# Performance work log

Hardware: AMD Instinct MI355X
Metric: run time of the kernel (lower is better)

## Reference

```python
import jax, jax.numpy as jnp
import numpy as np

D_MODEL = 1024
N_HEADS = 16
HEAD_DIM = D_MODEL // N_HEADS
N_MEM = 16
EPS = 1e-5
ROPE_THETA = 10000.0


def layernorm(x, g, b):
    mu = jnp.mean(x, axis=-1, keepdims=True)
    var = jnp.mean(jnp.square(x - mu), axis=-1, keepdims=True)
    return (x - mu) * jax.lax.rsqrt(var + EPS) * g + b


def rope_cos_sin(seq_len, head_dim, dtype):
    inv_freq = 1.0 / (ROPE_THETA ** (jnp.arange(0, head_dim, 2, dtype=jnp.float32) / head_dim))
    pos = jnp.arange(seq_len, dtype=jnp.float32)
    freqs = pos[:, None] * inv_freq[None, :]            # [S, hd/2]
    emb = jnp.concatenate([freqs, freqs], axis=-1)       # [S, hd]
    return jnp.cos(emb).astype(dtype), jnp.sin(emb).astype(dtype)


def rotate_half(x):
    x1, x2 = jnp.split(x, 2, axis=-1)
    return jnp.concatenate([-x2, x1], axis=-1)


def setup_inputs() -> dict:
    key = jax.random.key(0)
    ks = jax.random.split(key, 8)
    B, T, D = 2, 2048, D_MODEL
    x = jax.random.normal(ks[0], (B, T, D), dtype=jnp.float32)
    memory_tokens = jax.random.normal(ks[1], (1, N_MEM, D), dtype=jnp.float32) * 0.02
    s = 1.0 / np.sqrt(D)
    qkv_w = jax.random.uniform(ks[2], (3 * D, D), minval=-s, maxval=s, dtype=jnp.float32)
    qkv_b = jax.random.uniform(ks[3], (3 * D,), minval=-s, maxval=s, dtype=jnp.float32)
    out_w = jax.random.uniform(ks[4], (D, D), minval=-s, maxval=s, dtype=jnp.float32)
    out_b = jax.random.uniform(ks[5], (D,), minval=-s, maxval=s, dtype=jnp.float32)
    norm_g = jnp.ones((D,), jnp.float32)
    norm_b = jnp.zeros((D,), jnp.float32)
    normm_g = jnp.ones((D,), jnp.float32)
    normm_b = jnp.zeros((D,), jnp.float32)
    return {"x": x, "memory_tokens": memory_tokens, "qkv_w": qkv_w, "qkv_b": qkv_b,
            "out_w": out_w, "out_b": out_b, "norm_g": norm_g, "norm_b": norm_b,
            "normm_g": normm_g, "normm_b": normm_b}


def reference(x, memory_tokens, qkv_w, qkv_b, out_w, out_b, norm_g, norm_b, normm_g, normm_b):
    B, T, D = x.shape
    S = N_MEM + T
    residual = x
    x_norm = layernorm(x, norm_g, norm_b)
    mem = layernorm(jnp.broadcast_to(memory_tokens, (B, N_MEM, D)), normm_g, normm_b)
    xm = jnp.concatenate([mem, x_norm], axis=1)                # [B, S, D]
    qkv = xm @ qkv_w.T + qkv_b                                 # [B, S, 3D]
    qkv = qkv.reshape(B, S, 3, N_HEADS, HEAD_DIM)
    q = jnp.transpose(qkv[:, :, 0], (0, 2, 1, 3))              # [B, H, S, hd]
    k = jnp.transpose(qkv[:, :, 1], (0, 2, 1, 3))
    v = jnp.transpose(qkv[:, :, 2], (0, 2, 1, 3))
    cos, sin = rope_cos_sin(S, HEAD_DIM, x.dtype)              # [S, hd]
    q = q * cos + rotate_half(q) * sin
    k = k * cos + rotate_half(k) * sin
    scale = 1.0 / np.sqrt(HEAD_DIM)
    scores = jnp.einsum("bhqd,bhkd->bhqk", q, k) * scale       # [B, H, S, S]
    causal = jnp.tril(jnp.ones((S, S), dtype=bool))
    scores = jnp.where(causal, scores, jnp.finfo(scores.dtype).min)
    attn = jax.nn.softmax(scores, axis=-1)
    out = jnp.einsum("bhqk,bhkd->bhqd", attn, v)               # [B, H, S, hd]
    out = jnp.transpose(out, (0, 2, 1, 3)).reshape(B, S, D)
    out = out @ out_w.T + out_b
    out = out[:, N_MEM:, :]
    return residual + out
```

## Files before the change

kernel.cpp:

```cpp
#include <hip/hip_runtime.h>
#include <cstdint>


using bf16 = __bf16;
typedef __attribute__((ext_vector_type(8))) __bf16 bf16x8;
typedef __attribute__((ext_vector_type(4))) __bf16 bf16x4;
typedef __attribute__((ext_vector_type(4))) float floatx4;

#define MFMA16(a, b, c) __builtin_amdgcn_mfma_f32_16x16x32_bf16(a, b, c, 0, 0, 0)

constexpr int SV = 2064;
constexpr int SP = 2112;
constexpr float LOG2_THETA = 13.287712379549449f;

__device__ __forceinline__ bool dt_is_bf16(const void* p) {
  return *(const uint32_t*)p == 0x3F803F80u;
}

struct f8 { float v[8]; };

__device__ __forceinline__ f8 load8(const void* p, size_t idx, bool bf) {
  f8 r;
  if (bf) {
    bf16x8 t = *(const bf16x8*)((const bf16*)p + idx);
#pragma unroll
    for (int j = 0; j < 8; ++j) r.v[j] = (float)t[j];
  } else {
    float4 a = *(const float4*)((const float*)p + idx);
    float4 b = *(const float4*)((const float*)p + idx + 4);
    r.v[0] = a.x; r.v[1] = a.y; r.v[2] = a.z; r.v[3] = a.w;
    r.v[4] = b.x; r.v[5] = b.y; r.v[6] = b.z; r.v[7] = b.w;
  }
  return r;
}

__device__ __forceinline__ float ld1(const void* p, size_t idx, bool bf) {
  return bf ? (float)((const bf16*)p)[idx] : ((const float*)p)[idx];
}

__device__ __forceinline__ void load16_to_lds(const bf16* gptr, bf16* lptr) {
  auto* g = reinterpret_cast<const __attribute__((address_space(1))) uint32_t*>(
      reinterpret_cast<uintptr_t>(gptr));
  auto* l = reinterpret_cast<__attribute__((address_space(3))) uint32_t*>(
      reinterpret_cast<uintptr_t>(lptr));
  __builtin_amdgcn_global_load_lds(g, l, 16, 0, 0);
}

__global__ __launch_bounds__(256) void conv_w(
    const void* __restrict__ Wq, const void* __restrict__ Wo,
    const void* __restrict__ flagp, bf16* __restrict__ Wqb,
    bf16* __restrict__ Wob) {
  const bool bf = dt_is_bf16(flagp);
  const size_t i = ((size_t)blockIdx.x * 256 + threadIdx.x) * 8;
  const void* src;
  bf16* dst;
  size_t off;
  if (i < 3145728) { src = Wq; dst = Wqb; off = i; }
  else { src = Wo; dst = Wob; off = i - 3145728; }
  const f8 v = load8(src, off, bf);
  bf16x8 o;
#pragma unroll
  for (int j = 0; j < 8; ++j) o[j] = (bf16)v.v[j];
  *(bf16x8*)&dst[off] = o;
}

__global__ __launch_bounds__(256) void ln_all(
    const void* __restrict__ x, const void* __restrict__ mem,
    const void* __restrict__ ng, const void* __restrict__ nb,
    const void* __restrict__ mg, const void* __restrict__ mb,
    bf16* __restrict__ mem16, bf16* __restrict__ xln) {
  const bool bf = dt_is_bf16(ng);
  const int t = threadIdx.x, wid = t >> 6, lane = t & 63;
  const int row = blockIdx.x * 4 + wid;
  const void *src, *g, *bb;
  size_t soff;
  bf16* out;
  if (row < 16) {
    src = mem; soff = (size_t)row * 1024; g = mg; bb = mb;
    out = mem16 + (size_t)row * 1024;
  } else {
    src = x; soff = (size_t)(row - 16) * 1024; g = ng; bb = nb;
    out = xln + (size_t)(row - 16) * 1024;
  }
  const f8 v0 = load8(src, soff + lane * 8, bf);
  const f8 v1 = load8(src, soff + 512 + lane * 8, bf);
  float sum = 0.f, sq = 0.f;
#pragma unroll
  for (int j = 0; j < 8; ++j) { sum += v0.v[j]; sq += v0.v[j] * v0.v[j]; }
#pragma unroll
  for (int j = 0; j < 8; ++j) { sum += v1.v[j]; sq += v1.v[j] * v1.v[j]; }
#pragma unroll
  for (int off = 1; off < 64; off <<= 1) {
    sum += __shfl_xor(sum, off);
    sq += __shfl_xor(sq, off);
  }
  const float mu = sum * (1.0f / 1024.0f);
  const float var = sq * (1.0f / 1024.0f) - mu * mu;
  const float rstd = rsqrtf(var + 1e-5f);
  const f8 g0 = load8(g, lane * 8, bf), g1 = load8(g, 512 + lane * 8, bf);
  const f8 b0 = load8(bb, lane * 8, bf), b1 = load8(bb, 512 + lane * 8, bf);
  bf16x8 o0, o1;
#pragma unroll
  for (int j = 0; j < 8; ++j) {
    o0[j] = (bf16)((v0.v[j] - mu) * rstd * g0.v[j] + b0.v[j]);
    o1[j] = (bf16)((v1.v[j] - mu) * rstd * g1.v[j] + b1.v[j]);
  }
  *(bf16x8*)&out[lane * 8] = o0;
  *(bf16x8*)&out[512 + lane * 8] = o1;
}

__global__ __launch_bounds__(256) void gemm0_rope(
    const bf16* __restrict__ mem16, const bf16* __restrict__ xln,
    const bf16* __restrict__ Wqb, const void* __restrict__ bias,
    const void* __restrict__ flagp, bf16* __restrict__ Qg,
    bf16* __restrict__ Kg, bf16* __restrict__ Vg) {
  const bool bf = dt_is_bf16(flagp);
  __shared__ bf16 As[128 * 32];
  __shared__ bf16 Bs[128 * 32];
  const int t = threadIdx.x;
  const int row0 = blockIdx.x * 128;
  const int col0 = blockIdx.y * 128;
  const int wid = t >> 6, lane = t & 63, lr = lane & 15, lg = lane >> 4;
  const int wrow = (wid >> 1) * 64, wcol = (wid & 1) * 64;
  floatx4 acc[4][4] = {};

  const bf16* agp[2];
  const bf16* bgp[2];
#pragma unroll
  for (int c = 0; c < 2; ++c) {
    const int tt = c * 256 + t;
    int g = row0 + (tt >> 2);
    if (g > 4127) g = 4127;
    const int b2 = (g >= SV) ? 1 : 0;
    const int s = g - b2 * SV;
    const bf16* ap = (s < 16) ? (mem16 + (size_t)s * 1024)
                              : (xln + ((size_t)(b2 * 2048 + s - 16)) * 1024);
    agp[c] = ap + (tt & 3) * 8;
    bgp[c] = Wqb + (size_t)(col0 + (tt >> 2)) * 1024 + (tt & 3) * 8;
  }

  for (int k0 = 0; k0 < 1024; k0 += 32) {
    __syncthreads();
#pragma unroll
    for (int c = 0; c < 2; ++c) {
      const int tt = c * 256 + t;
      load16_to_lds(agp[c] + k0, &As[(tt & ~63) * 8]);
      load16_to_lds(bgp[c] + k0, &Bs[(tt & ~63) * 8]);
    }
    __syncthreads();
    bf16x8 af[4], bfr[4];
#pragma unroll
    for (int i = 0; i < 4; ++i) {
      af[i] = *(const bf16x8*)&As[(wrow + i * 16 + lr) * 32 + lg * 8];
      bfr[i] = *(const bf16x8*)&Bs[(wcol + i * 16 + lr) * 32 + lg * 8];
    }
#pragma unroll
    for (int mi = 0; mi < 4; ++mi)
#pragma unroll
      for (int ni = 0; ni < 4; ++ni)
        acc[mi][ni] = MFMA16(af[mi], bfr[ni], acc[mi][ni]);
  }

  const int colbase = col0 + wcol;
  const int part = colbase >> 10;
  const int h = (colbase >> 6) & 15;
  float f01[2];
  f01[0] = exp2f((float)lr * (-LOG2_THETA / 32.0f));
  f01[1] = exp2f((float)(16 + lr) * (-LOG2_THETA / 32.0f));

  if (part == 2) {
#pragma unroll
    for (int mi = 0; mi < 4; ++mi) {
      const int gq = row0 + wrow + mi * 16 + lg * 4;
      if (gq >= 2 * SV) continue;
      const int b2 = (gq >= SV) ? 1 : 0;
      const int pos = gq - b2 * SV;
      const size_t hb = (size_t)(b2 * 16 + h) * 64;
#pragma unroll
      for (int ni = 0; ni < 4; ++ni) {
        const int d = ni * 16 + lr;
        const float bc = ld1(bias, colbase + ni * 16 + lr, bf);
        bf16x4 vv;
#pragma unroll
        for (int r = 0; r < 4; ++r) vv[r] = (bf16)(acc[mi][ni][r] + bc);
        *(bf16x4*)&Vg[(hb + d) * SP + pos] = vv;
      }
    }
  } else {
    bf16* Dst = (part == 0) ? Qg : Kg;
    const float qs = (part == 0) ? 0.125f : 1.0f;
#pragma unroll
    for (int mi = 0; mi < 4; ++mi) {
#pragma unroll
      for (int r = 0; r < 4; ++r) {
        const int g = row0 + wrow + mi * 16 + lg * 4 + r;
        if (g >= 2 * SV) continue;
        const int b2 = (g >= SV) ? 1 : 0;
        const int pos = g - b2 * SV;
        bf16* drow = Dst + ((size_t)(b2 * 16 + h) * SP + pos) * 64;
#pragma unroll
        for (int a = 0; a < 2; ++a) {
          float c, sn;
          sincosf((float)pos * f01[a], &c, &sn);
          const float vlo = (acc[mi][a][r] + ld1(bias, colbase + a * 16 + lr, bf)) * qs;
          const float vhi = (acc[mi][a + 2][r] + ld1(bias, colbase + 32 + a * 16 + lr, bf)) * qs;
          drow[a * 16 + lr] = (bf16)(vlo * c - vhi * sn);
          drow[32 + a * 16 + lr] = (bf16)(vhi * c + vlo * sn);
        }
      }
    }
  }
}

__global__ __launch_bounds__(256) void flash3(
    const bf16* __restrict__ Qg, const bf16* __restrict__ Kg,
    const bf16* __restrict__ Vg, bf16* __restrict__ attn_out) {
  const int qt = 32 - blockIdx.x;
  const int bh = blockIdx.y;
  const int b = bh >> 4, h = bh & 15;
  const bf16* Qb = Qg + (size_t)bh * SP * 64;
  const bf16* Kb = Kg + (size_t)bh * SP * 64;
  const bf16* Vb = Vg + (size_t)bh * 64 * SP;

  const int t = threadIdx.x;
  const int wid = t >> 6, lane = t & 63, lr = lane & 15, lg = lane >> 4;
  const int qw0 = qt * 64 + wid * 16;

  __shared__ bf16 Ks[64 * 72];
  __shared__ bf16 Vt[64 * 64];
  __shared__ bf16 Ps[4][16 * 72];

  const int qs = qw0 + lr;
  bf16x8 qf0{}, qf1{};
  if (qs < SV) {
    qf0 = *(const bf16x8*)&Qb[(size_t)qs * 64 + lg * 8];
    qf1 = *(const bf16x8*)&Qb[(size_t)qs * 64 + 32 + lg * 8];
  }

  floatx4 o[4] = {};
  float lpart[4] = {};

  const int kr = t >> 2;
  const int kc = (t & 3) * 16;
  const int vd = t >> 2;
  const int vg0 = t & 3;
  const int vswz = ((vd & 7) ^ ((vd >> 4) & 3)) << 3;

  bf16x8 kA, kB, vA, vB;
  kA = *(const bf16x8*)&Kb[(size_t)kr * 64 + kc];
  kB = *(const bf16x8*)&Kb[(size_t)kr * 64 + kc + 8];
  vA = *(const bf16x8*)&Vb[(size_t)vd * SP + vg0 * 8];
  vB = *(const bf16x8*)&Vb[(size_t)vd * SP + (vg0 + 4) * 8];

  for (int kt = 0; kt <= qt; ++kt) {
    const int k0 = kt * 64;
    __syncthreads();
    *(bf16x8*)&Ks[kr * 72 + kc] = kA;
    *(bf16x8*)&Ks[kr * 72 + kc + 8] = kB;
    *(bf16x8*)&Vt[vd * 64 + ((vg0 << 3) ^ vswz)] = vA;
    *(bf16x8*)&Vt[vd * 64 + (((vg0 + 4) << 3) ^ vswz)] = vB;
    __syncthreads();
    if (kt < qt) {
      const int kn = k0 + 64;
      kA = *(const bf16x8*)&Kb[(size_t)(kn + kr) * 64 + kc];
      kB = *(const bf16x8*)&Kb[(size_t)(kn + kr) * 64 + kc + 8];
      vA = *(const bf16x8*)&Vb[(size_t)vd * SP + kn + vg0 * 8];
      vB = *(const bf16x8*)&Vb[(size_t)vd * SP + kn + (vg0 + 4) * 8];
    }

    floatx4 c[4] = {};
#pragma unroll
    for (int j2 = 0; j2 < 4; ++j2) {
      const bf16x8 kfa = *(const bf16x8*)&Ks[(j2 * 16 + lr) * 72 + lg * 8];
      const bf16x8 kfb = *(const bf16x8*)&Ks[(j2 * 16 + lr) * 72 + 32 + lg * 8];
      c[j2] = MFMA16(qf0, kfa, c[j2]);
      c[j2] = MFMA16(qf1, kfb, c[j2]);
    }

    const bool nm = (k0 + 63 > qw0);
#pragma unroll
    for (int r = 0; r < 4; ++r) {
      const int row = qw0 + lg * 4 + r;
      bf16* psr = &Ps[wid][(lg * 4 + r) * 72];
      float ls = 0.f;
#pragma unroll
      for (int j2 = 0; j2 < 4; ++j2) {
        float s = c[j2][r];
        if (nm && (k0 + j2 * 16 + lr > row)) s = -1e30f;
        const float p = __expf(s);
        ls += p;
        psr[j2 * 16 + lr] = (bf16)p;
      }
      lpart[r] += ls;
    }
    asm volatile("s_waitcnt lgkmcnt(0)" ::: "memory");
#pragma unroll
    for (int cc = 0; cc < 2; ++cc) {
      const bf16x8 pf = *(const bf16x8*)&Ps[wid][lr * 72 + cc * 32 + lg * 8];
#pragma unroll
      for (int dt = 0; dt < 4; ++dt) {
        const int key8 = (cc * 32 + lg * 8) ^ ((((lr & 7) ^ dt)) << 3);
        const bf16x8 vf = *(const bf16x8*)&Vt[(dt * 16 + lr) * 64 + key8];
        o[dt] = MFMA16(pf, vf, o[dt]);
      }
    }
  }

#pragma unroll
  for (int r = 0; r < 4; ++r) {
    float l = lpart[r];
    l += __shfl_xor(l, 1);
    l += __shfl_xor(l, 2);
    l += __shfl_xor(l, 4);
    l += __shfl_xor(l, 8);
    const int s = qw0 + lg * 4 + r;
    if (s < 16 || s >= SV) continue;
    const float inv = 1.0f / l;
    const size_t rowoff = ((size_t)(b * 2048 + s - 16)) * 1024 + h * 64;
#pragma unroll
    for (int dt = 0; dt < 4; ++dt)
      attn_out[rowoff + dt * 16 + lr] = (bf16)(o[dt][r] * inv);
  }
}

__global__ __launch_bounds__(256) void gemm1_proj(
    const bf16* __restrict__ A, const bf16* __restrict__ Wob,
    const void* __restrict__ bias, const void* __restrict__ x,
    const void* __restrict__ flagp, void* __restrict__ outp) {
  const bool bf = dt_is_bf16(flagp);
  __shared__ bf16 As[128 * 32];
  __shared__ bf16 Bs[128 * 32];
  const int t = threadIdx.x;
  const int row0 = blockIdx.x * 128;
  const int col0 = blockIdx.y * 128;
  const int wid = t >> 6, lane = t & 63, lr = lane & 15, lg = lane >> 4;
  const int wrow = (wid >> 1) * 64, wcol = (wid & 1) * 64;
  floatx4 acc[4][4] = {};

  const bf16* agp[2];
  const bf16* bgp[2];
#pragma unroll
  for (int c = 0; c < 2; ++c) {
    const int tt = c * 256 + t;
    agp[c] = A + (size_t)(row0 + (tt >> 2)) * 1024 + (tt & 3) * 8;
    bgp[c] = Wob + (size_t)(col0 + (tt >> 2)) * 1024 + (tt & 3) * 8;
  }

  for (int k0 = 0; k0 < 1024; k0 += 32) {
    __syncthreads();
#pragma unroll
    for (int c = 0; c < 2; ++c) {
      const int tt = c * 256 + t;
      load16_to_lds(agp[c] + k0, &As[(tt & ~63) * 8]);
      load16_to_lds(bgp[c] + k0, &Bs[(tt & ~63) * 8]);
    }
    __syncthreads();
    bf16x8 af[4], bfr[4];
#pragma unroll
    for (int i = 0; i < 4; ++i) {
      af[i] = *(const bf16x8*)&As[(wrow + i * 16 + lr) * 32 + lg * 8];
      bfr[i] = *(const bf16x8*)&Bs[(wcol + i * 16 + lr) * 32 + lg * 8];
    }
#pragma unroll
    for (int mi = 0; mi < 4; ++mi)
#pragma unroll
      for (int ni = 0; ni < 4; ++ni)
        acc[mi][ni] = MFMA16(af[mi], bfr[ni], acc[mi][ni]);
  }

#pragma unroll
  for (int mi = 0; mi < 4; ++mi) {
#pragma unroll
    for (int r = 0; r < 4; ++r) {
      const int row = row0 + wrow + mi * 16 + lg * 4 + r;
#pragma unroll
      for (int ni = 0; ni < 4; ++ni) {
        const int col = col0 + wcol + ni * 16 + lr;
        const size_t idx = (size_t)row * 1024 + col;
        const float v = acc[mi][ni][r] + ld1(bias, col, bf) + ld1(x, idx, bf);
        if (bf)
          ((bf16*)outp)[idx] = (bf16)v;
        else
          ((float*)outp)[idx] = v;
      }
    }
  }
}

extern "C" void kernel_launch(void* const* d_in, const int* in_sizes, int n_in,
                              void* d_out, int out_size, void* d_ws, size_t ws_size,
                              hipStream_t stream) {
  const void* x = d_in[0];
  const void* mem = d_in[1];
  const void* qkvw = d_in[2];
  const void* qkvb = d_in[3];
  const void* outw = d_in[4];
  const void* outb = d_in[5];
  const void* ng = d_in[6];
  const void* nb = d_in[7];
  const void* mg = d_in[8];
  const void* mb = d_in[9];

  char* ws = (char*)d_ws;
  bf16* mem16 = (bf16*)(ws);
  bf16* xln = (bf16*)(ws + 32768);
  bf16* Qg = (bf16*)(ws + 8421376);
  bf16* Kg = (bf16*)(ws + 17072128);
  bf16* Vg = (bf16*)(ws + 25722880);
  bf16* Wqb = (bf16*)(ws + 34373632);
  bf16* Wob = (bf16*)(ws + 40665088);
  bf16* attn = xln;

  conv_w<<<2048, 256, 0, stream>>>(qkvw, outw, ng, Wqb, Wob);
  ln_all<<<1028, 256, 0, stream>>>(x, mem, ng, nb, mg, mb, mem16, xln);
  gemm0_rope<<<dim3(33, 24), 256, 0, stream>>>(mem16, xln, Wqb, qkvb, ng,
                                               Qg, Kg, Vg);
  flash3<<<dim3(33, 32), 256, 0, stream>>>(Qg, Kg, Vg, attn);
  gemm1_proj<<<dim3(32, 8), 256, 0, stream>>>(attn, Wob, outb, x, ng, d_out);
}
```

Before: 240.8 us.

## Fuse all five kernels into one persistent megakernel with grid barriers

Merges weight conversion, layernorm, QKV GEMM with RoPE, flash attention and output projection into one persistent kernel of 1024 blocks. The phases are separated by atomic-counter grid barriers, with a memset resetting the counters. The aim is to remove the launch gaps and tails between the separate kernels. In exchange it relies on all 1024 blocks being co-resident (launch bounds of 4 blocks per CU) to avoid deadlock. The spin loop has a cap, and the static grid-stride assignment can leave phases load-imbalanced, notably the triangular causal attention.

```diff
diff --git a/kernel.cpp b/kernel.cpp
--- a/kernel.cpp
+++ b/kernel.cpp
@@ -46,342 +46,358 @@
   __builtin_amdgcn_global_load_lds(g, l, 16, 0, 0);
 }
 
-__global__ __launch_bounds__(256) void conv_w(
-    const void* __restrict__ Wq, const void* __restrict__ Wo,
-    const void* __restrict__ flagp, bf16* __restrict__ Wqb,
-    bf16* __restrict__ Wob) {
-  const bool bf = dt_is_bf16(flagp);
-  const size_t i = ((size_t)blockIdx.x * 256 + threadIdx.x) * 8;
-  const void* src;
-  bf16* dst;
-  size_t off;
-  if (i < 3145728) { src = Wq; dst = Wqb; off = i; }
-  else { src = Wo; dst = Wob; off = i - 3145728; }
-  const f8 v = load8(src, off, bf);
-  bf16x8 o;
-#pragma unroll
-  for (int j = 0; j < 8; ++j) o[j] = (bf16)v.v[j];
-  *(bf16x8*)&dst[off] = o;
-}
-
-__global__ __launch_bounds__(256) void ln_all(
+__device__ __forceinline__ void gbar(uint32_t* c) {
+  __syncthreads();
+  if (threadIdx.x == 0) {
+    __threadfence();
+    __hip_atomic_fetch_add(c, 1u, __ATOMIC_ACQ_REL, __HIP_MEMORY_SCOPE_AGENT);
+    uint32_t cap = 0;
+    while (__hip_atomic_load(c, __ATOMIC_ACQUIRE, __HIP_MEMORY_SCOPE_AGENT) <
+               gridDim.x &&
+           ++cap < 2000000u) {
+      __builtin_amdgcn_s_sleep(16);
+    }
+    __threadfence();
+  }
+  __syncthreads();
+}
+
+__global__ __launch_bounds__(256, 4) void mega(
     const void* __restrict__ x, const void* __restrict__ mem,
     const void* __restrict__ ng, const void* __restrict__ nb,
     const void* __restrict__ mg, const void* __restrict__ mb,
-    bf16* __restrict__ mem16, bf16* __restrict__ xln) {
+    const void* __restrict__ Wq, const void* __restrict__ Wo,
+    const void* __restrict__ qkvb, const void* __restrict__ outb,
+    bf16* __restrict__ mem16, bf16* __restrict__ xln,
+    bf16* __restrict__ Wqb, bf16* __restrict__ Wob,
+    bf16* __restrict__ Qg, bf16* __restrict__ Kg, bf16* __restrict__ Vg,
+    void* __restrict__ outp, uint32_t* __restrict__ bar) {
+  __shared__ __align__(16) char smem[26624];
   const bool bf = dt_is_bf16(ng);
-  const int t = threadIdx.x, wid = t >> 6, lane = t & 63;
-  const int row = blockIdx.x * 4 + wid;
-  const void *src, *g, *bb;
-  size_t soff;
-  bf16* out;
-  if (row < 16) {
-    src = mem; soff = (size_t)row * 1024; g = mg; bb = mb;
-    out = mem16 + (size_t)row * 1024;
-  } else {
-    src = x; soff = (size_t)(row - 16) * 1024; g = ng; bb = nb;
-    out = xln + (size_t)(row - 16) * 1024;
-  }
-  const f8 v0 = load8(src, soff + lane * 8, bf);
-  const f8 v1 = load8(src, soff + 512 + lane * 8, bf);
-  float sum = 0.f, sq = 0.f;
-#pragma unroll
-  for (int j = 0; j < 8; ++j) { sum += v0.v[j]; sq += v0.v[j] * v0.v[j]; }
-#pragma unroll
-  for (int j = 0; j < 8; ++j) { sum += v1.v[j]; sq += v1.v[j] * v1.v[j]; }
-#pragma unroll
-  for (int off = 1; off < 64; off <<= 1) {
-    sum += __shfl_xor(sum, off);
-    sq += __shfl_xor(sq, off);
-  }
-  const float mu = sum * (1.0f / 1024.0f);
-  const float var = sq * (1.0f / 1024.0f) - mu * mu;
-  const float rstd = rsqrtf(var + 1e-5f);
-  const f8 g0 = load8(g, lane * 8, bf), g1 = load8(g, 512 + lane * 8, bf);
-  const f8 b0 = load8(bb, lane * 8, bf), b1 = load8(bb, 512 + lane * 8, bf);
-  bf16x8 o0, o1;
-#pragma unroll
-  for (int j = 0; j < 8; ++j) {
-    o0[j] = (bf16)((v0.v[j] - mu) * rstd * g0.v[j] + b0.v[j]);
-    o1[j] = (bf16)((v1.v[j] - mu) * rstd * g1.v[j] + b1.v[j]);
-  }
-  *(bf16x8*)&out[lane * 8] = o0;
-  *(bf16x8*)&out[512 + lane * 8] = o1;
-}
-
-__global__ __launch_bounds__(256) void gemm0_rope(
-    const bf16* __restrict__ mem16, const bf16* __restrict__ xln,
-    const bf16* __restrict__ Wqb, const void* __restrict__ bias,
-    const void* __restrict__ flagp, bf16* __restrict__ Qg,
-    bf16* __restrict__ Kg, bf16* __restrict__ Vg) {
-  const bool bf = dt_is_bf16(flagp);
-  __shared__ bf16 As[128 * 32];
-  __shared__ bf16 Bs[128 * 32];
-  const int t = threadIdx.x;
-  const int row0 = blockIdx.x * 128;
-  const int col0 = blockIdx.y * 128;
-  const int wid = t >> 6, lane = t & 63, lr = lane & 15, lg = lane >> 4;
-  const int wrow = (wid >> 1) * 64, wcol = (wid & 1) * 64;
-  floatx4 acc[4][4] = {};
-
-  const bf16* agp[2];
-  const bf16* bgp[2];
-#pragma unroll
-  for (int c = 0; c < 2; ++c) {
-    const int tt = c * 256 + t;
-    int g = row0 + (tt >> 2);
-    if (g > 4127) g = 4127;
-    const int b2 = (g >= SV) ? 1 : 0;
-    const int s = g - b2 * SV;
-    const bf16* ap = (s < 16) ? (mem16 + (size_t)s * 1024)
-                              : (xln + ((size_t)(b2 * 2048 + s - 16)) * 1024);
-    agp[c] = ap + (tt & 3) * 8;
-    bgp[c] = Wqb + (size_t)(col0 + (tt >> 2)) * 1024 + (tt & 3) * 8;
-  }
-
-  for (int k0 = 0; k0 < 1024; k0 += 32) {
-    __syncthreads();
-#pragma unroll
-    for (int c = 0; c < 2; ++c) {
-      const int tt = c * 256 + t;
-      load16_to_lds(agp[c] + k0, &As[(tt & ~63) * 8]);
-      load16_to_lds(bgp[c] + k0, &Bs[(tt & ~63) * 8]);
-    }
-    __syncthreads();
-    bf16x8 af[4], bfr[4];
-#pragma unroll
-    for (int i = 0; i < 4; ++i) {
-      af[i] = *(const bf16x8*)&As[(wrow + i * 16 + lr) * 32 + lg * 8];
-      bfr[i] = *(const bf16x8*)&Bs[(wcol + i * 16 + lr) * 32 + lg * 8];
-    }
-#pragma unroll
-    for (int mi = 0; mi < 4; ++mi)
-#pragma unroll
-      for (int ni = 0; ni < 4; ++ni)
-        acc[mi][ni] = MFMA16(af[mi], bfr[ni], acc[mi][ni]);
-  }
-
-  const int colbase = col0 + wcol;
-  const int part = colbase >> 10;
-  const int h = (colbase >> 6) & 15;
-  float f01[2];
-  f01[0] = exp2f((float)lr * (-LOG2_THETA / 32.0f));
-  f01[1] = exp2f((float)(16 + lr) * (-LOG2_THETA / 32.0f));
-
-  if (part == 2) {
-#pragma unroll
-    for (int mi = 0; mi < 4; ++mi) {
-      const int gq = row0 + wrow + mi * 16 + lg * 4;
-      if (gq >= 2 * SV) continue;
-      const int b2 = (gq >= SV) ? 1 : 0;
-      const int pos = gq - b2 * SV;
-      const size_t hb = (size_t)(b2 * 16 + h) * 64;
-#pragma unroll
-      for (int ni = 0; ni < 4; ++ni) {
-        const int d = ni * 16 + lr;
-        const float bc = ld1(bias, colbase + ni * 16 + lr, bf);
-        bf16x4 vv;
-#pragma unroll
-        for (int r = 0; r < 4; ++r) vv[r] = (bf16)(acc[mi][ni][r] + bc);
-        *(bf16x4*)&Vg[(hb + d) * SP + pos] = vv;
-      }
-    }
-  } else {
-    bf16* Dst = (part == 0) ? Qg : Kg;
-    const float qs = (part == 0) ? 0.125f : 1.0f;
-#pragma unroll
-    for (int mi = 0; mi < 4; ++mi) {
-#pragma unroll
-      for (int r = 0; r < 4; ++r) {
-        const int g = row0 + wrow + mi * 16 + lg * 4 + r;
-        if (g >= 2 * SV) continue;
-        const int b2 = (g >= SV) ? 1 : 0;
-        const int pos = g - b2 * SV;
-        bf16* drow = Dst + ((size_t)(b2 * 16 + h) * SP + pos) * 64;
-#pragma unroll
-        for (int a = 0; a < 2; ++a) {
-          float c, sn;
-          sincosf((float)pos * f01[a], &c, &sn);
-          const float vlo = (acc[mi][a][r] + ld1(bias, colbase + a * 16 + lr, bf)) * qs;
-          const float vhi = (acc[mi][a + 2][r] + ld1(bias, colbase + 32 + a * 16 + lr, bf)) * qs;
-          drow[a * 16 + lr] = (bf16)(vlo * c - vhi * sn);
-          drow[32 + a * 16 + lr] = (bf16)(vhi * c + vlo * sn);
-        }
-      }
-    }
-  }
-}
-
-__global__ __launch_bounds__(256) void flash3(
-    const bf16* __restrict__ Qg, const bf16* __restrict__ Kg,
-    const bf16* __restrict__ Vg, bf16* __restrict__ attn_out) {
-  const int qt = 32 - blockIdx.x;
-  const int bh = blockIdx.y;
-  const int b = bh >> 4, h = bh & 15;
-  const bf16* Qb = Qg + (size_t)bh * SP * 64;
-  const bf16* Kb = Kg + (size_t)bh * SP * 64;
-  const bf16* Vb = Vg + (size_t)bh * 64 * SP;
-
   const int t = threadIdx.x;
   const int wid = t >> 6, lane = t & 63, lr = lane & 15, lg = lane >> 4;
-  const int qw0 = qt * 64 + wid * 16;
-
-  __shared__ bf16 Ks[64 * 72];
-  __shared__ bf16 Vt[64 * 64];
-  __shared__ bf16 Ps[4][16 * 72];
-
-  const int qs = qw0 + lr;
-  bf16x8 qf0{}, qf1{};
-  if (qs < SV) {
-    qf0 = *(const bf16x8*)&Qb[(size_t)qs * 64 + lg * 8];
-    qf1 = *(const bf16x8*)&Qb[(size_t)qs * 64 + 32 + lg * 8];
-  }
-
-  floatx4 o[4] = {};
-  float lpart[4] = {};
-
-  const int kr = t >> 2;
-  const int kc = (t & 3) * 16;
-  const int vd = t >> 2;
-  const int vg0 = t & 3;
-  const int vswz = ((vd & 7) ^ ((vd >> 4) & 3)) << 3;
-
-  bf16x8 kA, kB, vA, vB;
-  kA = *(const bf16x8*)&Kb[(size_t)kr * 64 + kc];
-  kB = *(const bf16x8*)&Kb[(size_t)kr * 64 + kc + 8];
-  vA = *(const bf16x8*)&Vb[(size_t)vd * SP + vg0 * 8];
-  vB = *(const bf16x8*)&Vb[(size_t)vd * SP + (vg0 + 4) * 8];
-
-  for (int kt = 0; kt <= qt; ++kt) {
-    const int k0 = kt * 64;
-    __syncthreads();
-    *(bf16x8*)&Ks[kr * 72 + kc] = kA;
-    *(bf16x8*)&Ks[kr * 72 + kc + 8] = kB;
-    *(bf16x8*)&Vt[vd * 64 + ((vg0 << 3) ^ vswz)] = vA;
-    *(bf16x8*)&Vt[vd * 64 + (((vg0 + 4) << 3) ^ vswz)] = vB;
-    __syncthreads();
-    if (kt < qt) {
-      const int kn = k0 + 64;
-      kA = *(const bf16x8*)&Kb[(size_t)(kn + kr) * 64 + kc];
-      kB = *(const bf16x8*)&Kb[(size_t)(kn + kr) * 64 + kc + 8];
-      vA = *(const bf16x8*)&Vb[(size_t)vd * SP + kn + vg0 * 8];
-      vB = *(const bf16x8*)&Vb[(size_t)vd * SP + kn + (vg0 + 4) * 8];
-    }
-
-    floatx4 c[4] = {};
-#pragma unroll
-    for (int j2 = 0; j2 < 4; ++j2) {
-      const bf16x8 kfa = *(const bf16x8*)&Ks[(j2 * 16 + lr) * 72 + lg * 8];
-      const bf16x8 kfb = *(const bf16x8*)&Ks[(j2 * 16 + lr) * 72 + 32 + lg * 8];
-      c[j2] = MFMA16(qf0, kfa, c[j2]);
-      c[j2] = MFMA16(qf1, kfb, c[j2]);
-    }
-
-    const bool nm = (k0 + 63 > qw0);
-#pragma unroll
-    for (int r = 0; r < 4; ++r) {
-      const int row = qw0 + lg * 4 + r;
-      bf16* psr = &Ps[wid][(lg * 4 + r) * 72];
-      float ls = 0.f;
-#pragma unroll
-      for (int j2 = 0; j2 < 4; ++j2) {
-        float s = c[j2][r];
-        if (nm && (k0 + j2 * 16 + lr > row)) s = -1e30f;
-        const float p = __expf(s);
-        ls += p;
-        psr[j2 * 16 + lr] = (bf16)p;
-      }
-      lpart[r] += ls;
-    }
-    asm volatile("s_waitcnt lgkmcnt(0)" ::: "memory");
-#pragma unroll
-    for (int cc = 0; cc < 2; ++cc) {
-      const bf16x8 pf = *(const bf16x8*)&Ps[wid][lr * 72 + cc * 32 + lg * 8];
-#pragma unroll
-      for (int dt = 0; dt < 4; ++dt) {
-        const int key8 = (cc * 32 + lg * 8) ^ ((((lr & 7) ^ dt)) << 3);
-        const bf16x8 vf = *(const bf16x8*)&Vt[(dt * 16 + lr) * 64 + key8];
-        o[dt] = MFMA16(pf, vf, o[dt]);
-      }
-    }
-  }
-
-#pragma unroll
-  for (int r = 0; r < 4; ++r) {
-    float l = lpart[r];
-    l += __shfl_xor(l, 1);
-    l += __shfl_xor(l, 2);
-    l += __shfl_xor(l, 4);
-    l += __shfl_xor(l, 8);
-    const int s = qw0 + lg * 4 + r;
-    if (s < 16 || s >= SV) continue;
-    const float inv = 1.0f / l;
-    const size_t rowoff = ((size_t)(b * 2048 + s - 16)) * 1024 + h * 64;
-#pragma unroll
-    for (int dt = 0; dt < 4; ++dt)
-      attn_out[rowoff + dt * 16 + lr] = (bf16)(o[dt][r] * inv);
-  }
-}
-
-__global__ __launch_bounds__(256) void gemm1_proj(
-    const bf16* __restrict__ A, const bf16* __restrict__ Wob,
-    const void* __restrict__ bias, const void* __restrict__ x,
-    const void* __restrict__ flagp, void* __restrict__ outp) {
-  const bool bf = dt_is_bf16(flagp);
-  __shared__ bf16 As[128 * 32];
-  __shared__ bf16 Bs[128 * 32];
-  const int t = threadIdx.x;
-  const int row0 = blockIdx.x * 128;
-  const int col0 = blockIdx.y * 128;
-  const int wid = t >> 6, lane = t & 63, lr = lane & 15, lg = lane >> 4;
-  const int wrow = (wid >> 1) * 64, wcol = (wid & 1) * 64;
-  floatx4 acc[4][4] = {};
-
-  const bf16* agp[2];
-  const bf16* bgp[2];
-#pragma unroll
-  for (int c = 0; c < 2; ++c) {
-    const int tt = c * 256 + t;
-    agp[c] = A + (size_t)(row0 + (tt >> 2)) * 1024 + (tt & 3) * 8;
-    bgp[c] = Wob + (size_t)(col0 + (tt >> 2)) * 1024 + (tt & 3) * 8;
-  }
-
-  for (int k0 = 0; k0 < 1024; k0 += 32) {
-    __syncthreads();
-#pragma unroll
-    for (int c = 0; c < 2; ++c) {
-      const int tt = c * 256 + t;
-      load16_to_lds(agp[c] + k0, &As[(tt & ~63) * 8]);
-      load16_to_lds(bgp[c] + k0, &Bs[(tt & ~63) * 8]);
-    }
-    __syncthreads();
-    bf16x8 af[4], bfr[4];
-#pragma unroll
-    for (int i = 0; i < 4; ++i) {
-      af[i] = *(const bf16x8*)&As[(wrow + i * 16 + lr) * 32 + lg * 8];
-      bfr[i] = *(const bf16x8*)&Bs[(wcol + i * 16 + lr) * 32 + lg * 8];
-    }
-#pragma unroll
-    for (int mi = 0; mi < 4; ++mi)
-#pragma unroll
-      for (int ni = 0; ni < 4; ++ni)
-        acc[mi][ni] = MFMA16(af[mi], bfr[ni], acc[mi][ni]);
-  }
-
-#pragma unroll
-  for (int mi = 0; mi < 4; ++mi) {
-#pragma unroll
-    for (int r = 0; r < 4; ++r) {
-      const int row = row0 + wrow + mi * 16 + lg * 4 + r;
-#pragma unroll
-      for (int ni = 0; ni < 4; ++ni) {
-        const int col = col0 + wcol + ni * 16 + lr;
-        const size_t idx = (size_t)row * 1024 + col;
-        const float v = acc[mi][ni][r] + ld1(bias, col, bf) + ld1(x, idx, bf);
-        if (bf)
-          ((bf16*)outp)[idx] = (bf16)v;
-        else
-          ((float*)outp)[idx] = v;
+
+  for (int vb = blockIdx.x; vb < 3076; vb += 1024) {
+    if (vb < 2048) {
+      const size_t i = ((size_t)vb * 256 + t) * 8;
+      const void* src;
+      bf16* dst;
+      size_t off;
+      if (i < 3145728) { src = Wq; dst = Wqb; off = i; }
+      else { src = Wo; dst = Wob; off = i - 3145728; }
+      const f8 v = load8(src, off, bf);
+      bf16x8 o;
+#pragma unroll
+      for (int j = 0; j < 8; ++j) o[j] = (bf16)v.v[j];
+      *(bf16x8*)&dst[off] = o;
+      continue;
+    }
+    const int row = (vb - 2048) * 4 + wid;
+    const void *src, *g, *bb;
+    size_t soff;
+    bf16* out;
+    if (row < 16) {
+      src = mem; soff = (size_t)row * 1024; g = mg; bb = mb;
+      out = mem16 + (size_t)row * 1024;
+    } else {
+      src = x; soff = (size_t)(row - 16) * 1024; g = ng; bb = nb;
+      out = xln + (size_t)(row - 16) * 1024;
+    }
+    const f8 v0 = load8(src, soff + lane * 8, bf);
+    const f8 v1 = load8(src, soff + 512 + lane * 8, bf);
+    float sum = 0.f, sq = 0.f;
+#pragma unroll
+    for (int j = 0; j < 8; ++j) { sum += v0.v[j]; sq += v0.v[j] * v0.v[j]; }
+#pragma unroll
+    for (int j = 0; j < 8; ++j) { sum += v1.v[j]; sq += v1.v[j] * v1.v[j]; }
+#pragma unroll
+    for (int off = 1; off < 64; off <<= 1) {
+      sum += __shfl_xor(sum, off);
+      sq += __shfl_xor(sq, off);
+    }
+    const float mu = sum * (1.0f / 1024.0f);
+    const float var = sq * (1.0f / 1024.0f) - mu * mu;
+    const float rstd = rsqrtf(var + 1e-5f);
+    const f8 g0 = load8(g, lane * 8, bf), g1 = load8(g, 512 + lane * 8, bf);
+    const f8 b0 = load8(bb, lane * 8, bf), b1 = load8(bb, 512 + lane * 8, bf);
+    bf16x8 o0, o1;
+#pragma unroll
+    for (int j = 0; j < 8; ++j) {
+      o0[j] = (bf16)((v0.v[j] - mu) * rstd * g0.v[j] + b0.v[j]);
+      o1[j] = (bf16)((v1.v[j] - mu) * rstd * g1.v[j] + b1.v[j]);
+    }
+    *(bf16x8*)&out[lane * 8] = o0;
+    *(bf16x8*)&out[512 + lane * 8] = o1;
+  }
+  gbar(bar + 0);
+
+  {
+    bf16* As = (bf16*)smem;
+    bf16* Bs = As + 128 * 32;
+    const int wrow = (wid >> 1) * 64, wcol = (wid & 1) * 64;
+    for (int vb = blockIdx.x; vb < 792; vb += 1024) {
+      const int row0 = (vb % 33) * 128;
+      const int col0 = (vb / 33) * 128;
+      floatx4 acc[4][4] = {};
+
+      const bf16* agp[2];
+      const bf16* bgp[2];
+#pragma unroll
+      for (int c = 0; c < 2; ++c) {
+        const int tt = c * 256 + t;
+        int g = row0 + (tt >> 2);
+        if (g > 4127) g = 4127;
+        const int b2 = (g >= SV) ? 1 : 0;
+        const int s = g - b2 * SV;
+        const bf16* ap = (s < 16) ? (mem16 + (size_t)s * 1024)
+                                  : (xln + ((size_t)(b2 * 2048 + s - 16)) * 1024);
+        agp[c] = ap + (tt & 3) * 8;
+        bgp[c] = Wqb + (size_t)(col0 + (tt >> 2)) * 1024 + (tt & 3) * 8;
+      }
+
+      for (int k0 = 0; k0 < 1024; k0 += 32) {
+        __syncthreads();
+#pragma unroll
+        for (int c = 0; c < 2; ++c) {
+          const int tt = c * 256 + t;
+          load16_to_lds(agp[c] + k0, &As[(tt & ~63) * 8]);
+          load16_to_lds(bgp[c] + k0, &Bs[(tt & ~63) * 8]);
+        }
+        __syncthreads();
+        bf16x8 af[4], bfr[4];
+#pragma unroll
+        for (int i = 0; i < 4; ++i) {
+          af[i] = *(const bf16x8*)&As[(wrow + i * 16 + lr) * 32 + lg * 8];
+          bfr[i] = *(const bf16x8*)&Bs[(wcol + i * 16 + lr) * 32 + lg * 8];
+        }
+#pragma unroll
+        for (int mi = 0; mi < 4; ++mi)
+#pragma unroll
+          for (int ni = 0; ni < 4; ++ni)
+            acc[mi][ni] = MFMA16(af[mi], bfr[ni], acc[mi][ni]);
+      }
+
+      const int colbase = col0 + wcol;
+      const int part = colbase >> 10;
+      const int h = (colbase >> 6) & 15;
+      float f01[2];
+      f01[0] = exp2f((float)lr * (-LOG2_THETA / 32.0f));
+      f01[1] = exp2f((float)(16 + lr) * (-LOG2_THETA / 32.0f));
+
+      if (part == 2) {
+#pragma unroll
+        for (int mi = 0; mi < 4; ++mi) {
+          const int gq = row0 + wrow + mi * 16 + lg * 4;
+          if (gq >= 2 * SV) continue;
+          const int b2 = (gq >= SV) ? 1 : 0;
+          const int pos = gq - b2 * SV;
+          const size_t hb = (size_t)(b2 * 16 + h) * 64;
+#pragma unroll
+          for (int ni = 0; ni < 4; ++ni) {
+            const int d = ni * 16 + lr;
+            const float bc = ld1(qkvb, colbase + ni * 16 + lr, bf);
+            bf16x4 vv;
+#pragma unroll
+            for (int r = 0; r < 4; ++r) vv[r] = (bf16)(acc[mi][ni][r] + bc);
+            *(bf16x4*)&Vg[(hb + d) * SP + pos] = vv;
+          }
+        }
+      } else {
+        bf16* Dst = (part == 0) ? Qg : Kg;
+        const float qs = (part == 0) ? 0.125f : 1.0f;
+#pragma unroll
+        for (int mi = 0; mi < 4; ++mi) {
+#pragma unroll
+          for (int r = 0; r < 4; ++r) {
+            const int g = row0 + wrow + mi * 16 + lg * 4 + r;
+            if (g >= 2 * SV) continue;
+            const int b2 = (g >= SV) ? 1 : 0;
+            const int pos = g - b2 * SV;
+            bf16* drow = Dst + ((size_t)(b2 * 16 + h) * SP + pos) * 64;
+#pragma unroll
+            for (int a = 0; a < 2; ++a) {
+              float c, sn;
+              sincosf((float)pos * f01[a], &c, &sn);
+              const float vlo =
+                  (acc[mi][a][r] + ld1(qkvb, colbase + a * 16 + lr, bf)) * qs;
+              const float vhi =
+                  (acc[mi][a + 2][r] + ld1(qkvb, colbase + 32 + a * 16 + lr, bf)) * qs;
+              drow[a * 16 + lr] = (bf16)(vlo * c - vhi * sn);
+              drow[32 + a * 16 + lr] = (bf16)(vhi * c + vlo * sn);
+            }
+          }
+        }
+      }
+    }
+  }
+  gbar(bar + 1);
+
+  {
+    bf16* Ks = (bf16*)smem;
+    bf16* Vt = Ks + 64 * 72;
+    bf16* Psw = Vt + 64 * 64 + wid * (16 * 72);
+    bf16* attn_out = xln;
+    const int kr = t >> 2;
+    const int kc = (t & 3) * 16;
+    const int vd = t >> 2;
+    const int vg0 = t & 3;
+    const int vswz = ((vd & 7) ^ ((vd >> 4) & 3)) << 3;
+
+    for (int vb = blockIdx.x; vb < 1056; vb += 1024) {
+      const int qt = 32 - (vb >> 5);
+      const int bh = vb & 31;
+      const int b = bh >> 4, h = bh & 15;
+      const bf16* Qb = Qg + (size_t)bh * SP * 64;
+      const bf16* Kb = Kg + (size_t)bh * SP * 64;
+      const bf16* Vb = Vg + (size_t)bh * 64 * SP;
+      const int qw0 = qt * 64 + wid * 16;
+
+      const int qs = qw0 + lr;
+      bf16x8 qf0{}, qf1{};
+      if (qs < SV) {
+        qf0 = *(const bf16x8*)&Qb[(size_t)qs * 64 + lg * 8];
+        qf1 = *(const bf16x8*)&Qb[(size_t)qs * 64 + 32 + lg * 8];
+      }
+
+      floatx4 o[4] = {};
+      float lpart[4] = {};
+
+      bf16x8 kA, kB, vA, vB;
+      kA = *(const bf16x8*)&Kb[(size_t)kr * 64 + kc];
+      kB = *(const bf16x8*)&Kb[(size_t)kr * 64 + kc + 8];
+      vA = *(const bf16x8*)&Vb[(size_t)vd * SP + vg0 * 8];
+      vB = *(const bf16x8*)&Vb[(size_t)vd * SP + (vg0 + 4) * 8];
+
+      for (int kt = 0; kt <= qt; ++kt) {
+        const int k0 = kt * 64;
+        __syncthreads();
+        *(bf16x8*)&Ks[kr * 72 + kc] = kA;
+        *(bf16x8*)&Ks[kr * 72 + kc + 8] = kB;
+        *(bf16x8*)&Vt[vd * 64 + ((vg0 << 3) ^ vswz)] = vA;
+        *(bf16x8*)&Vt[vd * 64 + (((vg0 + 4) << 3) ^ vswz)] = vB;
+        __syncthreads();
+        if (kt < qt) {
+          const int kn = k0 + 64;
+          kA = *(const bf16x8*)&Kb[(size_t)(kn + kr) * 64 + kc];
+          kB = *(const bf16x8*)&Kb[(size_t)(kn + kr) * 64 + kc + 8];
+          vA = *(const bf16x8*)&Vb[(size_t)vd * SP + kn + vg0 * 8];
+          vB = *(const bf16x8*)&Vb[(size_t)vd * SP + kn + (vg0 + 4) * 8];
+        }
+
+        floatx4 c[4] = {};
+#pragma unroll
+        for (int j2 = 0; j2 < 4; ++j2) {
+          const bf16x8 kfa = *(const bf16x8*)&Ks[(j2 * 16 + lr) * 72 + lg * 8];
+          const bf16x8 kfb = *(const bf16x8*)&Ks[(j2 * 16 + lr) * 72 + 32 + lg * 8];
+          c[j2] = MFMA16(qf0, kfa, c[j2]);
+          c[j2] = MFMA16(qf1, kfb, c[j2]);
+        }
+
+        const bool nm = (k0 + 63 > qw0);
+#pragma unroll
+        for (int r = 0; r < 4; ++r) {
+          const int row = qw0 + lg * 4 + r;
+          bf16* psr = &Psw[(lg * 4 + r) * 72];
+          float ls = 0.f;
+#pragma unroll
+          for (int j2 = 0; j2 < 4; ++j2) {
+            float s = c[j2][r];
+            if (nm && (k0 + j2 * 16 + lr > row)) s = -1e30f;
+            const float p = __expf(s);
+            ls += p;
+            psr[j2 * 16 + lr] = (bf16)p;
+          }
+          lpart[r] += ls;
+        }
+        asm volatile("s_waitcnt lgkmcnt(0)" ::: "memory");
+#pragma unroll
+        for (int cc = 0; cc < 2; ++cc) {
+          const bf16x8 pf = *(const bf16x8*)&Psw[lr * 72 + cc * 32 + lg * 8];
+#pragma unroll
+          for (int dt = 0; dt < 4; ++dt) {
+            const int key8 = (cc * 32 + lg * 8) ^ ((((lr & 7) ^ dt)) << 3);
+            const bf16x8 vf = *(const bf16x8*)&Vt[(dt * 16 + lr) * 64 + key8];
+            o[dt] = MFMA16(pf, vf, o[dt]);
+          }
+        }
+      }
+
+#pragma unroll
+      for (int r = 0; r < 4; ++r) {
+        float l = lpart[r];
+        l += __shfl_xor(l, 1);
+        l += __shfl_xor(l, 2);
+        l += __shfl_xor(l, 4);
+        l += __shfl_xor(l, 8);
+        const int s = qw0 + lg * 4 + r;
+        if (s < 16 || s >= SV) continue;
+        const float inv = 1.0f / l;
+        const size_t rowoff = ((size_t)(b * 2048 + s - 16)) * 1024 + h * 64;
+#pragma unroll
+        for (int dt = 0; dt < 4; ++dt)
+          attn_out[rowoff + dt * 16 + lr] = (bf16)(o[dt][r] * inv);
+      }
+    }
+  }
+  gbar(bar + 2);
+
+  {
+    bf16* As = (bf16*)smem;
+    bf16* Bs = As + 128 * 32;
+    const bf16* A = xln;
+    const int wrow = (wid >> 1) * 64, wcol = (wid & 1) * 64;
+    for (int vb = blockIdx.x; vb < 256; vb += 1024) {
+      const int row0 = (vb % 32) * 128;
+      const int col0 = (vb / 32) * 128;
+      floatx4 acc[4][4] = {};
+
+      const bf16* agp[2];
+      const bf16* bgp[2];
+#pragma unroll
+      for (int c = 0; c < 2; ++c) {
+        const int tt = c * 256 + t;
+        agp[c] = A + (size_t)(row0 + (tt >> 2)) * 1024 + (tt & 3) * 8;
+        bgp[c] = Wob + (size_t)(col0 + (tt >> 2)) * 1024 + (tt & 3) * 8;
+      }
+
+      for (int k0 = 0; k0 < 1024; k0 += 32) {
+        __syncthreads();
+#pragma unroll
+        for (int c = 0; c < 2; ++c) {
+          const int tt = c * 256 + t;
+          load16_to_lds(agp[c] + k0, &As[(tt & ~63) * 8]);
+          load16_to_lds(bgp[c] + k0, &Bs[(tt & ~63) * 8]);
+        }
+        __syncthreads();
+        bf16x8 af[4], bfr[4];
+#pragma unroll
+        for (int i = 0; i < 4; ++i) {
+          af[i] = *(const bf16x8*)&As[(wrow + i * 16 + lr) * 32 + lg * 8];
+          bfr[i] = *(const bf16x8*)&Bs[(wcol + i * 16 + lr) * 32 + lg * 8];
+        }
+#pragma unroll
+        for (int mi = 0; mi < 4; ++mi)
+#pragma unroll
+          for (int ni = 0; ni < 4; ++ni)
+            acc[mi][ni] = MFMA16(af[mi], bfr[ni], acc[mi][ni]);
+      }
+
+#pragma unroll
+      for (int mi = 0; mi < 4; ++mi) {
+#pragma unroll
+        for (int r = 0; r < 4; ++r) {
+          const int row = row0 + wrow + mi * 16 + lg * 4 + r;
+#pragma unroll
+          for (int ni = 0; ni < 4; ++ni) {
+            const int col = col0 + wcol + ni * 16 + lr;
+            const size_t idx = (size_t)row * 1024 + col;
+            const float v = acc[mi][ni][r] + ld1(outb, col, bf) + ld1(x, idx, bf);
+            if (bf)
+              ((bf16*)outp)[idx] = (bf16)v;
+            else
+              ((float*)outp)[idx] = v;
+          }
+        }
       }
     }
   }
@@ -409,12 +425,9 @@
   bf16* Vg = (bf16*)(ws + 25722880);
   bf16* Wqb = (bf16*)(ws + 34373632);
   bf16* Wob = (bf16*)(ws + 40665088);
-  bf16* attn = xln;
-
-  conv_w<<<2048, 256, 0, stream>>>(qkvw, outw, ng, Wqb, Wob);
-  ln_all<<<1028, 256, 0, stream>>>(x, mem, ng, nb, mg, mb, mem16, xln);
-  gemm0_rope<<<dim3(33, 24), 256, 0, stream>>>(mem16, xln, Wqb, qkvb, ng,
-                                               Qg, Kg, Vg);
-  flash3<<<dim3(33, 32), 256, 0, stream>>>(Qg, Kg, Vg, attn);
-  gemm1_proj<<<dim3(32, 8), 256, 0, stream>>>(attn, Wob, outb, x, ng, d_out);
-}
+  uint32_t* bar = (uint32_t*)(ws + 42762240);
+
+  hipMemsetAsync(bar, 0, 64, stream);
+  mega<<<1024, 256, 0, stream>>>(x, mem, ng, nb, mg, mb, qkvw, outw, qkvb, outb,
+                                 mem16, xln, Wqb, Wob, Qg, Kg, Vg, d_out, bar);
+}
```

Result: slower. 930.8 us (+286.5%).
